# Optimization experiments

Hardware: AMD Instinct MI355X
Metric: run time of the kernel (lower is better)

Reference implementation:

```python
import jax, jax.numpy as jnp
import numpy as np

BN_EPS = 1e-5
K = 3  # kernel_size
G = 4  # num_groups


def setup_inputs() -> dict:
    key = jax.random.key(0)
    ks = jax.random.split(key, 8)
    B, C, H, W = 16, 192, 96, 96
    R = C // 4
    return {
        "x": jax.random.normal(ks[0], (B, C, H, W), jnp.float32),
        "cam_w1": jax.random.normal(ks[1], (R, C), jnp.float32) * 0.05,
        "cam_w2": jax.random.normal(ks[2], (C, R), jnp.float32) * 0.05,
        "proj_w1": jax.random.normal(ks[3], (R, C), jnp.float32) * 0.05,
        "bn_gamma": jnp.ones((R,), jnp.float32),
        "bn_beta": jnp.zeros((R,), jnp.float32),
        "proj_w2": jax.random.normal(ks[4], (G * C, R), jnp.float32) * 0.05,
        "adk_weight": jax.random.normal(ks[5], (G, C, K, K), jnp.float32) * 0.02,
    }


def reference(x, cam_w1, cam_w2, proj_w1, bn_gamma, bn_beta, proj_w2, adk_weight):
    B, C, H, W = x.shape

    # ---- CAM: theta = sigmoid(fc(avgpool1(x)) + fc(maxpool1(x))) -> [B, C]
    def fc(v):  # v: [B, C]
        h = jax.nn.relu(v @ cam_w1.T)  # [B, C//4]
        return h @ cam_w2.T            # [B, C]

    avg = x.mean(axis=(2, 3))
    mx = x.max(axis=(2, 3))
    theta = jax.nn.sigmoid(fc(avg) + fc(mx))  # [B, C]

    # ---- AdaptiveDynamicKernel: dynamic per-(sample,channel) 3x3 filters
    # AdaptiveAvgPool2d(3): H, W divisible by 3 -> uniform pooling
    pooled = x.reshape(B, C, K, H // K, K, W // K).mean(axis=(3, 5))  # [B,C,3,3]
    h = jnp.einsum('bchw,rc->brhw', pooled, proj_w1)  # [B, C//4, 3, 3]
    # BatchNorm2d (eval, running_mean=0, running_var=1)
    scale_bn = bn_gamma / jnp.sqrt(1.0 + BN_EPS)
    h = jax.nn.relu(h * scale_bn[None, :, None, None] + bn_beta[None, :, None, None])
    s = jnp.einsum('brhw,or->bohw', h, proj_w2)  # [B, G*C, 3, 3]
    s = s.reshape(B, G, C, K, K)
    s = jax.nn.softmax(s, axis=1)
    weight = jnp.sum(s * adk_weight[None], axis=1)  # [B, C, 3, 3]

    # ---- central-difference correction
    w_sum = weight.sum(axis=(2, 3))         # [B, C]
    w_center = weight[:, :, K // 2, K // 2]  # [B, C]
    delta = w_sum - theta * w_center
    weight_s = weight.at[:, :, K // 2, K // 2].add(-delta)

    # ---- grouped depthwise conv, groups = B*C
    kernel = weight_s.reshape(B * C, 1, K, K)
    xin = x.reshape(1, B * C, H, W)
    out = jax.lax.conv_general_dilated(
        xin, kernel,
        window_strides=(1, 1),
        padding=[(K // 2, K // 2), (K // 2, K // 2)],
        dimension_numbers=('NCHW', 'OIHW', 'NCHW'),
        feature_group_count=B * C,
    )
    return out.reshape(B, C, H, W)
```

## Files before the change

### kernel.cpp

```cpp
#include <hip/hip_runtime.h>
#include <math.h>

#define CCH   192
#define RCH   48
#define NB    16
#define HW    9216
#define BCTOT (NB*CCH)

__global__ __launch_bounds__(256) void k_stats(const float* __restrict__ x,
                                               float* __restrict__ avg,
                                               float* __restrict__ mx,
                                               float* __restrict__ pooled)
{
    int bc = blockIdx.x;
    const float4* p4 = (const float4*)(x + (size_t)bc * HW);
    int t = threadIdx.x;
    float ps[9];
    float m = -INFINITY;
#pragma unroll
    for (int k = 0; k < 9; ++k) {
        int kr = k / 3, kc = k % 3;
        int row = kr * 32 + (t >> 3);
        int wq  = kc * 8  + (t & 7);
        float4 v = p4[row * 24 + wq];
        ps[k] = v.x + v.y + v.z + v.w;
        m = fmaxf(m, fmaxf(fmaxf(v.x, v.y), fmaxf(v.z, v.w)));
    }
#pragma unroll
    for (int off = 32; off > 0; off >>= 1) {
#pragma unroll
        for (int k = 0; k < 9; ++k) ps[k] += __shfl_down(ps[k], off);
        m = fmaxf(m, __shfl_down(m, off));
    }
    __shared__ float red[4][10];
    int wid = t >> 6, lane = t & 63;
    if (lane == 0) {
#pragma unroll
        for (int k = 0; k < 9; ++k) red[wid][k] = ps[k];
        red[wid][9] = m;
    }
    __syncthreads();
    if (t == 0) {
        float tot = 0.f;
#pragma unroll
        for (int k = 0; k < 9; ++k) {
            float pk = red[0][k] + red[1][k] + red[2][k] + red[3][k];
            pooled[bc * 9 + k] = pk * (1.0f / 1024.0f);
            tot += pk;
        }
        float mm = fmaxf(fmaxf(red[0][9], red[1][9]),
                         fmaxf(red[2][9], red[3][9]));
        avg[bc] = tot * (1.0f / (float)HW);
        mx[bc]  = mm;
    }
}

__global__ __launch_bounds__(256) void k_coeff(
    const float* __restrict__ avg, const float* __restrict__ mx,
    const float* __restrict__ pooled,
    const float* __restrict__ cam_w1, const float* __restrict__ cam_w2,
    const float* __restrict__ proj_w1,
    const float* __restrict__ bn_gamma, const float* __restrict__ bn_beta,
    const float* __restrict__ proj_w2, const float* __restrict__ adk,
    float* __restrict__ theta, float* __restrict__ wgt)
{
    int b = blockIdx.x;
    int t = threadIdx.x;
    __shared__ float s_av[CCH], s_mx[CCH], s_pool[CCH * 9];
    __shared__ float s_h1p[96], s_h1[RCH], s_hh[RCH * 9];
    if (t < CCH) { s_av[t] = avg[b * CCH + t]; s_mx[t] = mx[b * CCH + t]; }
    for (int i = t; i < CCH * 9; i += 256) s_pool[i] = pooled[b * CCH * 9 + i];
    __syncthreads();
    if (t < 96) {
        int r = t % 48, sel = t / 48;
        const float* src = sel ? s_mx : s_av;
        const float* w = cam_w1 + r * CCH;
        float acc = 0.f;
        for (int c = 0; c < CCH; ++c) acc += src[c] * w[c];
        s_h1p[sel * 48 + r] = fmaxf(acc, 0.f);
    }
    __syncthreads();
    if (t < RCH) s_h1[t] = s_h1p[t] + s_h1p[48 + t];
    __syncthreads();
    if (t < CCH) {
        const float* w = cam_w2 + t * RCH;
        float acc = 0.f;
        for (int r = 0; r < RCH; ++r) acc += s_h1[r] * w[r];
        theta[b * CCH + t] = 1.0f / (1.0f + expf(-acc));
    }
    float bn_s = 1.0f / sqrtf(1.0f + 1e-5f);
    for (int i = t; i < RCH * 9; i += 256) {
        int r = i / 9, k = i % 9;
        const float* w = proj_w1 + r * CCH;
        float acc = 0.f;
        for (int c = 0; c < CCH; ++c) acc += s_pool[c * 9 + k] * w[c];
        float val = acc * (bn_gamma[r] * bn_s) + bn_beta[r];
        s_hh[i] = fmaxf(val, 0.f);
    }
    __syncthreads();
    for (int i = t; i < CCH * 9; i += 256) {
        int c = i / 9, k = i % 9;
        float sg[4];
#pragma unroll
        for (int g = 0; g < 4; ++g) {
            const float* w = proj_w2 + (size_t)(g * CCH + c) * RCH;
            float acc = 0.f;
            for (int r = 0; r < RCH; ++r) acc += s_hh[r * 9 + k] * w[r];
            sg[g] = acc;
        }
        float mxv = fmaxf(fmaxf(sg[0], sg[1]), fmaxf(sg[2], sg[3]));
        float e[4];
        float sum = 0.f;
#pragma unroll
        for (int g = 0; g < 4; ++g) { e[g] = expf(sg[g] - mxv); sum += e[g]; }
        float inv = 1.0f / sum;
        float acc = 0.f;
#pragma unroll
        for (int g = 0; g < 4; ++g)
            acc += (e[g] * inv) * adk[(size_t)(g * CCH + c) * 9 + k];
        wgt[b * CCH * 9 + i] = acc;
    }
}

__global__ __launch_bounds__(256) void k_conv(
    const float* __restrict__ x, const float* __restrict__ wgt,
    const float* __restrict__ theta, float* __restrict__ out)
{
    int t = threadIdx.x;
    int wid = t >> 6, lane = t & 63;
    int plane = blockIdx.x * 4 + wid;
    int rg = lane >> 3, cs = lane & 7;
    int rbase = rg * 12 - 1;

    float wr[9];
    float wsum = 0.f;
#pragma unroll
    for (int k = 0; k < 9; ++k) { wr[k] = wgt[plane * 9 + k]; wsum += wr[k]; }
    float th = theta[plane];
    wr[4] = wr[4] * (1.f + th) - wsum;

    const float4* p4 = (const float4*)(x + (size_t)plane * HW);
    float4* o4p = (float4*)(out + (size_t)plane * HW);

    float acc[3][12];
#pragma unroll
    for (int i = 0; i <= 13; ++i) {
        int r = rbase + i;
        bool inr = (r >= 0) && (r < 96);
        float4 a0, a1, a2;
        if (inr) {
            const float4* prow = p4 + r * 24 + cs * 3;
            a0 = prow[0]; a1 = prow[1]; a2 = prow[2];
        } else {
            a0 = make_float4(0.f, 0.f, 0.f, 0.f);
            a1 = a0; a2 = a0;
        }
        float lv = __shfl_up(a2.w, 1);
        float rv = __shfl_down(a0.x, 1);
        float w[14];
        w[0] = (cs == 0) ? 0.f : lv;
        w[1] = a0.x; w[2] = a0.y; w[3] = a0.z; w[4] = a0.w;
        w[5] = a1.x; w[6] = a1.y; w[7] = a1.z; w[8] = a1.w;
        w[9] = a2.x; w[10] = a2.y; w[11] = a2.z; w[12] = a2.w;
        w[13] = (cs == 7) ? 0.f : rv;

        if (i <= 11) {
#pragma unroll
            for (int j = 0; j < 12; ++j)
                acc[i % 3][j] = wr[0] * w[j] + wr[1] * w[j + 1] + wr[2] * w[j + 2];
        }
        if (i >= 1 && i <= 12) {
#pragma unroll
            for (int j = 0; j < 12; ++j)
                acc[(i - 1) % 3][j] += wr[3] * w[j] + wr[4] * w[j + 1] + wr[5] * w[j + 2];
        }
        if (i >= 2) {
            const int s = (i - 2) % 3;
#pragma unroll
            for (int j = 0; j < 12; ++j)
                acc[s][j] += wr[6] * w[j] + wr[7] * w[j + 1] + wr[8] * w[j + 2];
            int orow = rbase + i - 1;
            float4* od = o4p + orow * 24 + cs * 3;
            od[0] = make_float4(acc[s][0], acc[s][1], acc[s][2], acc[s][3]);
            od[1] = make_float4(acc[s][4], acc[s][5], acc[s][6], acc[s][7]);
            od[2] = make_float4(acc[s][8], acc[s][9], acc[s][10], acc[s][11]);
        }
    }
}

extern "C" void kernel_launch(void* const* d_in, const int* in_sizes, int n_in,
                              void* d_out, int out_size, void* d_ws, size_t ws_size,
                              hipStream_t stream) {
    const float* x        = (const float*)d_in[0];
    const float* cam_w1   = (const float*)d_in[1];
    const float* cam_w2   = (const float*)d_in[2];
    const float* proj_w1  = (const float*)d_in[3];
    const float* bn_gamma = (const float*)d_in[4];
    const float* bn_beta  = (const float*)d_in[5];
    const float* proj_w2  = (const float*)d_in[6];
    const float* adk      = (const float*)d_in[7];
    float* out = (float*)d_out;
    float* ws  = (float*)d_ws;

    float* avg    = ws;
    float* mx     = ws + 3072;
    float* pooled = ws + 6144;
    float* theta  = ws + 33792;
    float* wgt    = ws + 36864;

    k_stats <<<BCTOT, 256, 0, stream>>>(x, avg, mx, pooled);
    k_coeff <<<NB,    256, 0, stream>>>(avg, mx, pooled, cam_w1, cam_w2,
                                        proj_w1, bn_gamma, bn_beta,
                                        proj_w2, adk, theta, wgt);
    k_conv  <<<BCTOT / 4, 256, 0, stream>>>(x, wgt, theta, out);
}
```

Measured before the change: 95.34 us.

## Interleave conv column mapping for coalesced float4 access and halve rows per thread

```diff
diff --git a/kernel.cpp b/kernel.cpp
--- a/kernel.cpp
+++ b/kernel.cpp
@@ -128,9 +128,12 @@
 {
     int t = threadIdx.x;
     int wid = t >> 6, lane = t & 63;
-    int plane = blockIdx.x * 4 + wid;
-    int rg = lane >> 3, cs = lane & 7;
-    int rbase = rg * 12 - 1;
+    int plane = blockIdx.x * 2 + (wid >> 1);
+    int half  = wid & 1;
+    int rgL = lane >> 3, cs = lane & 7;
+    int rbase = half * 48 + rgL * 6 - 1;
+    int lane7 = (lane & 56) | 7;
+    int lane0 = (lane & 56);
 
     float wr[9];
     float wsum = 0.f;
@@ -142,48 +145,62 @@
     const float4* p4 = (const float4*)(x + (size_t)plane * HW);
     float4* o4p = (float4*)(out + (size_t)plane * HW);
 
-    float acc[3][12];
-#pragma unroll
-    for (int i = 0; i <= 13; ++i) {
+    float acc[3][3][4];
+#pragma unroll
+    for (int i = 0; i < 8; ++i) {
         int r = rbase + i;
         bool inr = (r >= 0) && (r < 96);
         float4 a0, a1, a2;
         if (inr) {
-            const float4* prow = p4 + r * 24 + cs * 3;
-            a0 = prow[0]; a1 = prow[1]; a2 = prow[2];
+            const float4* prow = p4 + r * 24 + cs;
+            a0 = prow[0]; a1 = prow[8]; a2 = prow[16];
         } else {
             a0 = make_float4(0.f, 0.f, 0.f, 0.f);
             a1 = a0; a2 = a0;
         }
-        float lv = __shfl_up(a2.w, 1);
-        float rv = __shfl_down(a0.x, 1);
-        float w[14];
-        w[0] = (cs == 0) ? 0.f : lv;
-        w[1] = a0.x; w[2] = a0.y; w[3] = a0.z; w[4] = a0.w;
-        w[5] = a1.x; w[6] = a1.y; w[7] = a1.z; w[8] = a1.w;
-        w[9] = a2.x; w[10] = a2.y; w[11] = a2.z; w[12] = a2.w;
-        w[13] = (cs == 7) ? 0.f : rv;
-
-        if (i <= 11) {
-#pragma unroll
-            for (int j = 0; j < 12; ++j)
-                acc[i % 3][j] = wr[0] * w[j] + wr[1] * w[j + 1] + wr[2] * w[j + 2];
-        }
-        if (i >= 1 && i <= 12) {
-#pragma unroll
-            for (int j = 0; j < 12; ++j)
-                acc[(i - 1) % 3][j] += wr[3] * w[j] + wr[4] * w[j + 1] + wr[5] * w[j + 2];
+        float lw0 = __shfl_up(a0.w, 1), lw1 = __shfl_up(a1.w, 1), lw2 = __shfl_up(a2.w, 1);
+        float rw0 = __shfl_down(a0.x, 1), rw1 = __shfl_down(a1.x, 1), rw2 = __shfl_down(a2.x, 1);
+        float lb1 = __shfl(a0.w, lane7, 64);
+        float lb2 = __shfl(a1.w, lane7, 64);
+        float rb0 = __shfl(a1.x, lane0, 64);
+        float rb1 = __shfl(a2.x, lane0, 64);
+        float w6[3][6];
+        w6[0][0] = (cs == 0) ? 0.f : lw0;
+        w6[1][0] = (cs == 0) ? lb1 : lw1;
+        w6[2][0] = (cs == 0) ? lb2 : lw2;
+        w6[0][5] = (cs == 7) ? rb0 : rw0;
+        w6[1][5] = (cs == 7) ? rb1 : rw1;
+        w6[2][5] = (cs == 7) ? 0.f : rw2;
+        w6[0][1] = a0.x; w6[0][2] = a0.y; w6[0][3] = a0.z; w6[0][4] = a0.w;
+        w6[1][1] = a1.x; w6[1][2] = a1.y; w6[1][3] = a1.z; w6[1][4] = a1.w;
+        w6[2][1] = a2.x; w6[2][2] = a2.y; w6[2][3] = a2.z; w6[2][4] = a2.w;
+
+        if (i <= 5) {
+#pragma unroll
+            for (int j = 0; j < 3; ++j)
+#pragma unroll
+                for (int c = 0; c < 4; ++c)
+                    acc[i % 3][j][c] = wr[0] * w6[j][c] + wr[1] * w6[j][c + 1] + wr[2] * w6[j][c + 2];
+        }
+        if (i >= 1 && i <= 6) {
+#pragma unroll
+            for (int j = 0; j < 3; ++j)
+#pragma unroll
+                for (int c = 0; c < 4; ++c)
+                    acc[(i - 1) % 3][j][c] += wr[3] * w6[j][c] + wr[4] * w6[j][c + 1] + wr[5] * w6[j][c + 2];
         }
         if (i >= 2) {
             const int s = (i - 2) % 3;
 #pragma unroll
-            for (int j = 0; j < 12; ++j)
-                acc[s][j] += wr[6] * w[j] + wr[7] * w[j + 1] + wr[8] * w[j + 2];
+            for (int j = 0; j < 3; ++j)
+#pragma unroll
+                for (int c = 0; c < 4; ++c)
+                    acc[s][j][c] += wr[6] * w6[j][c] + wr[7] * w6[j][c + 1] + wr[8] * w6[j][c + 2];
             int orow = rbase + i - 1;
-            float4* od = o4p + orow * 24 + cs * 3;
-            od[0] = make_float4(acc[s][0], acc[s][1], acc[s][2], acc[s][3]);
-            od[1] = make_float4(acc[s][4], acc[s][5], acc[s][6], acc[s][7]);
-            od[2] = make_float4(acc[s][8], acc[s][9], acc[s][10], acc[s][11]);
+            float4* od = o4p + orow * 24 + cs;
+            od[0]  = make_float4(acc[s][0][0], acc[s][0][1], acc[s][0][2], acc[s][0][3]);
+            od[8]  = make_float4(acc[s][1][0], acc[s][1][1], acc[s][1][2], acc[s][1][3]);
+            od[16] = make_float4(acc[s][2][0], acc[s][2][1], acc[s][2][2], acc[s][2][3]);
         }
     }
 }
@@ -212,5 +229,5 @@
     k_coeff <<<NB,    256, 0, stream>>>(avg, mx, pooled, cam_w1, cam_w2,
                                         proj_w1, bn_gamma, bn_beta,
                                         proj_w2, adk, theta, wgt);
-    k_conv  <<<BCTOT / 4, 256, 0, stream>>>(x, wgt, theta, out);
-}
+    k_conv  <<<BCTOT / 2, 256, 0, stream>>>(x, wgt, theta, out);
+}
```

After: 94.18 us. About the same (-1.2%).

## Stage whole plane in LDS for depthwise conv, one plane per block

Applied to the files above, without the earlier changes.

```diff
diff --git a/kernel.cpp b/kernel.cpp
--- a/kernel.cpp
+++ b/kernel.cpp
@@ -126,11 +126,30 @@
     const float* __restrict__ x, const float* __restrict__ wgt,
     const float* __restrict__ theta, float* __restrict__ out)
 {
+    __shared__ __align__(16) float s_raw[4 + 98 * 100];
+    float* sx = s_raw + 4;
+    float4* sx4 = (float4*)sx;
+
+    int plane = blockIdx.x;
     int t = threadIdx.x;
-    int wid = t >> 6, lane = t & 63;
-    int plane = blockIdx.x * 4 + wid;
-    int rg = lane >> 3, cs = lane & 7;
-    int rbase = rg * 12 - 1;
+
+    if (t < 4) s_raw[t] = 0.f;
+    if (t < 200) {
+        int r = t / 100, c = t % 100;
+        sx[(r == 0 ? 0 : 97) * 100 + c] = 0.f;
+    }
+    for (int i = t; i < 384; i += 256) {
+        int r = i >> 2, j = i & 3;
+        sx[(r + 1) * 100 + 96 + j] = 0.f;
+    }
+
+    const float4* p4 = (const float4*)(x + (size_t)plane * HW);
+#pragma unroll
+    for (int i = 0; i < 9; ++i) {
+        int i4 = t + i * 256;
+        int row = i4 / 24, c4 = i4 % 24;
+        sx4[(row + 1) * 25 + c4] = p4[i4];
+    }
 
     float wr[9];
     float wsum = 0.f;
@@ -139,51 +158,50 @@
     float th = theta[plane];
     wr[4] = wr[4] * (1.f + th) - wsum;
 
-    const float4* p4 = (const float4*)(x + (size_t)plane * HW);
+    __syncthreads();
+
+    int rg = t >> 3, cs = t & 7;
     float4* o4p = (float4*)(out + (size_t)plane * HW);
 
-    float acc[3][12];
-#pragma unroll
-    for (int i = 0; i <= 13; ++i) {
-        int r = rbase + i;
-        bool inr = (r >= 0) && (r < 96);
-        float4 a0, a1, a2;
-        if (inr) {
-            const float4* prow = p4 + r * 24 + cs * 3;
-            a0 = prow[0]; a1 = prow[1]; a2 = prow[2];
-        } else {
-            a0 = make_float4(0.f, 0.f, 0.f, 0.f);
-            a1 = a0; a2 = a0;
-        }
-        float lv = __shfl_up(a2.w, 1);
-        float rv = __shfl_down(a0.x, 1);
-        float w[14];
-        w[0] = (cs == 0) ? 0.f : lv;
-        w[1] = a0.x; w[2] = a0.y; w[3] = a0.z; w[4] = a0.w;
-        w[5] = a1.x; w[6] = a1.y; w[7] = a1.z; w[8] = a1.w;
-        w[9] = a2.x; w[10] = a2.y; w[11] = a2.z; w[12] = a2.w;
-        w[13] = (cs == 7) ? 0.f : rv;
-
-        if (i <= 11) {
-#pragma unroll
-            for (int j = 0; j < 12; ++j)
-                acc[i % 3][j] = wr[0] * w[j] + wr[1] * w[j + 1] + wr[2] * w[j + 2];
-        }
-        if (i >= 1 && i <= 12) {
-#pragma unroll
-            for (int j = 0; j < 12; ++j)
-                acc[(i - 1) % 3][j] += wr[3] * w[j] + wr[4] * w[j + 1] + wr[5] * w[j + 2];
+    float acc[3][3][4];
+#pragma unroll
+    for (int i = 0; i < 5; ++i) {
+        int lr = 3 * rg + i;
+        float w6[3][6];
+#pragma unroll
+        for (int jb = 0; jb < 3; ++jb) {
+            int fc = cs + 8 * jb;
+            float4 a = sx4[lr * 25 + fc];
+            w6[jb][0] = sx[lr * 100 + 4 * fc - 1];
+            w6[jb][1] = a.x; w6[jb][2] = a.y; w6[jb][3] = a.z; w6[jb][4] = a.w;
+            w6[jb][5] = sx[lr * 100 + 4 * fc + 4];
+        }
+        if (i <= 2) {
+#pragma unroll
+            for (int jb = 0; jb < 3; ++jb)
+#pragma unroll
+                for (int c = 0; c < 4; ++c)
+                    acc[i][jb][c] = wr[0] * w6[jb][c] + wr[1] * w6[jb][c + 1] + wr[2] * w6[jb][c + 2];
+        }
+        if (i >= 1 && i <= 3) {
+#pragma unroll
+            for (int jb = 0; jb < 3; ++jb)
+#pragma unroll
+                for (int c = 0; c < 4; ++c)
+                    acc[i - 1][jb][c] += wr[3] * w6[jb][c] + wr[4] * w6[jb][c + 1] + wr[5] * w6[jb][c + 2];
         }
         if (i >= 2) {
-            const int s = (i - 2) % 3;
-#pragma unroll
-            for (int j = 0; j < 12; ++j)
-                acc[s][j] += wr[6] * w[j] + wr[7] * w[j + 1] + wr[8] * w[j + 2];
-            int orow = rbase + i - 1;
-            float4* od = o4p + orow * 24 + cs * 3;
-            od[0] = make_float4(acc[s][0], acc[s][1], acc[s][2], acc[s][3]);
-            od[1] = make_float4(acc[s][4], acc[s][5], acc[s][6], acc[s][7]);
-            od[2] = make_float4(acc[s][8], acc[s][9], acc[s][10], acc[s][11]);
+            const int s = i - 2;
+#pragma unroll
+            for (int jb = 0; jb < 3; ++jb)
+#pragma unroll
+                for (int c = 0; c < 4; ++c)
+                    acc[s][jb][c] += wr[6] * w6[jb][c] + wr[7] * w6[jb][c + 1] + wr[8] * w6[jb][c + 2];
+            int orow = 3 * rg + s;
+#pragma unroll
+            for (int jb = 0; jb < 3; ++jb)
+                o4p[orow * 24 + 8 * jb + cs] =
+                    make_float4(acc[s][jb][0], acc[s][jb][1], acc[s][jb][2], acc[s][jb][3]);
         }
     }
 }
@@ -212,5 +230,5 @@
     k_coeff <<<NB,    256, 0, stream>>>(avg, mx, pooled, cam_w1, cam_w2,
                                         proj_w1, bn_gamma, bn_beta,
                                         proj_w2, adk, theta, wgt);
-    k_conv  <<<BCTOT / 4, 256, 0, stream>>>(x, wgt, theta, out);
-}
+    k_conv  <<<BCTOT, 256, 0, stream>>>(x, wgt, theta, out);
+}
```

After: 98.90 us. +3.7%, slower.
